# Performance work log

Measured on AMD Instinct MI355X. Metric: run time of the kernel, lower is better.

Reference implementation:

```python
import jax, jax.numpy as jnp
import numpy as np

B, N, D = 4, 2048, 512
H, DH = 8, 64  # heads, dim_head; inner_dim = H*DH = 512
SCALE = DH ** -0.5


def setup_inputs() -> dict:
    key = jax.random.key(0)
    kx, kw = jax.random.split(key)
    x = jax.random.normal(kx, (B, N, D), dtype=jnp.float32)
    # torch Linear weight layout: [out_features=3*H*DH, in_features=D]
    W_qkv = jax.random.normal(kw, (3 * H * DH, D), dtype=jnp.float32) * 0.02
    return {"x": x, "W_qkv": W_qkv}


def reference(x, W_qkv):
    b, n, d = x.shape
    # qkv projection (no bias since qkv_bias=False)
    qkv = x @ W_qkv.T                                  # [b, n, 3*H*DH]
    qkv = qkv.reshape(b, n, 3, H, DH).transpose(2, 0, 3, 1, 4)  # [3, b, H, n, DH]
    q, k, v = qkv[0], qkv[1], qkv[2]
    # shifted query: q_cross[t] = q[t-1] for t>=1, q_cross[0] = q[0]
    q_cross = jnp.concatenate([q[:, :, :1, :], q[:, :, :-1, :]], axis=2)
    scores = jnp.einsum("bhqd,bhkd->bhqk", q_cross * SCALE, k)  # [b, H, n, n]
    attn = jax.nn.softmax(scores, axis=-1)
    out = jnp.einsum("bhqk,bhkd->bhqd", attn, v)       # [b, H, n, DH]
    out = out.transpose(0, 2, 1, 3).reshape(b, n, H * DH)
    # to_out is Dropout(0.0) -> identity in eval / p=0
    return out
```

## Files before the change

kernel.cpp:

```cpp
#include <hip/hip_runtime.h>
#include <hip/hip_bf16.h>
#include <stdint.h>

typedef __bf16 bf16_t;
typedef float floatx4 __attribute__((ext_vector_type(4)));
typedef __bf16 bf16x8 __attribute__((ext_vector_type(8)));
typedef __bf16 bf16x4 __attribute__((ext_vector_type(4)));

#define QSCALE 0.1803368801111204f

__device__ __forceinline__ void gl2lds16(const bf16_t* g, bf16_t* l) {
    __builtin_amdgcn_global_load_lds(
        (const __attribute__((address_space(1))) unsigned int*)g,
        (__attribute__((address_space(3))) unsigned int*)l,
        16, 0, 0);
}

__global__ __launch_bounds__(256) void convert_kernel(const float* __restrict__ x,
                                                      bf16_t* __restrict__ xb,
                                                      const float* __restrict__ w,
                                                      bf16_t* __restrict__ wb,
                                                      int nx4) {
    int i = blockIdx.x * 256 + threadIdx.x;
    const float* in; bf16_t* out; int j;
    if (i < nx4) { in = x; out = xb; j = i; }
    else         { in = w; out = wb; j = i - nx4; }
    float4 v = ((const float4*)in)[j];
    bf16x4 o;
    o.x = (bf16_t)v.x; o.y = (bf16_t)v.y; o.z = (bf16_t)v.z; o.w = (bf16_t)v.w;
    ((bf16x4*)out)[j] = o;
}

__global__ __launch_bounds__(256) void qkv_gemm(const bf16_t* __restrict__ X,
                                                const bf16_t* __restrict__ W,
                                                bf16_t* __restrict__ Q,
                                                bf16_t* __restrict__ K,
                                                bf16_t* __restrict__ Vt)
{
    __shared__ bf16_t As[128 * 64];
    __shared__ bf16_t Bs[128 * 64];

    const int tid  = threadIdx.x;
    const int wave = tid >> 6;
    const int lane = tid & 63;
    const int quad = lane >> 4;
    const int lrow = lane & 15;
    const int t7g  = lrow & 7;
    const int bm0 = blockIdx.x * 128;
    const int bn0 = blockIdx.y * 128;
    const int mw = (wave >> 1) * 64;
    const int nw = (wave & 1) * 64;
    const int wbase = tid & 192;

    floatx4 acc[4][4];
#pragma unroll
    for (int i = 0; i < 4; i++)
#pragma unroll
        for (int j = 0; j < 4; j++) acc[i][j] = (floatx4)0.0f;

#pragma unroll 1
    for (int kb = 0; kb < 8; ++kb) {
        const int k0 = kb * 64;
        __syncthreads();
#pragma unroll
        for (int r = 0; r < 4; ++r) {
            int c = r * 256 + tid;
            int row = c >> 3, kc = c & 7;
            int skc = kc ^ (row & 7);
            gl2lds16(X + (size_t)(bm0 + row) * 512 + k0 + skc * 8,
                     As + (size_t)(r * 256 + wbase) * 8);
        }
#pragma unroll
        for (int r = 0; r < 4; ++r) {
            int c = r * 256 + tid;
            int row = c >> 3, kc = c & 7;
            int skc = kc ^ (row & 7);
            gl2lds16(W + (size_t)(bn0 + row) * 512 + k0 + skc * 8,
                     Bs + (size_t)(r * 256 + wbase) * 8);
        }
        __syncthreads();
#pragma unroll
        for (int ks = 0; ks < 2; ++ks) {
            bf16x8 af[4], bfr[4];
#pragma unroll
            for (int mi = 0; mi < 4; mi++)
                af[mi] = *(const bf16x8*)(As + (mw + mi * 16 + lrow) * 64 + (((ks * 4 + quad) ^ t7g) << 3));
#pragma unroll
            for (int ni = 0; ni < 4; ni++)
                bfr[ni] = *(const bf16x8*)(Bs + (nw + ni * 16 + lrow) * 64 + (((ks * 4 + quad) ^ t7g) << 3));
#pragma unroll
            for (int mi = 0; mi < 4; mi++)
#pragma unroll
                for (int ni = 0; ni < 4; ni++)
                    acc[mi][ni] = __builtin_amdgcn_mfma_f32_16x16x32_bf16(af[mi], bfr[ni], acc[mi][ni], 0, 0, 0);
        }
    }

#pragma unroll
    for (int mi = 0; mi < 4; mi++) {
        int mbase = bm0 + mw + mi * 16 + quad * 4;
        int b = mbase >> 11, n = mbase & 2047;
#pragma unroll
        for (int ni = 0; ni < 4; ni++) {
            int o = bn0 + nw + ni * 16 + lrow;
            int s  = o >> 9;
            int h  = (o >> 6) & 7;
            int dh = o & 63;
            int bh = b * 8 + h;
            if (s == 2) {
                bf16x4 pv;
#pragma unroll
                for (int r = 0; r < 4; r++) pv[r] = (bf16_t)acc[mi][ni][r];
                *(bf16x4*)(Vt + ((size_t)bh * 64 + dh) * 2048 + n) = pv;
            } else if (s == 0) {
#pragma unroll
                for (int r = 0; r < 4; r++)
                    Q[((size_t)bh * 2048 + n + r) * 64 + dh] = (bf16_t)(acc[mi][ni][r] * QSCALE);
            } else {
#pragma unroll
                for (int r = 0; r < 4; r++)
                    K[((size_t)bh * 2048 + n + r) * 64 + dh] = (bf16_t)acc[mi][ni][r];
            }
        }
    }
}

__device__ __forceinline__ void stage_tile(const bf16_t* __restrict__ kb,
                                           const bf16_t* __restrict__ vb,
                                           int kt, bf16_t* ksbuf, bf16_t* vsbuf,
                                           int wave, int lane) {
#pragma unroll
    for (int part = 0; part < 2; ++part) {
        int ch  = part * 256 + wave * 64 + lane;
        int row = ch >> 3, cc = ch & 7;
        int scc = cc ^ (row & 7);
        bf16_t* ldst = ksbuf + (size_t)(part * 256 + wave * 64) * 8;
        gl2lds16(kb + ((size_t)(kt * 64 + row)) * 64 + scc * 8, ldst);
        bf16_t* ldst2 = vsbuf + (size_t)(part * 256 + wave * 64) * 8;
        gl2lds16(vb + (size_t)row * 2048 + kt * 64 + scc * 8, ldst2);
    }
}

__global__ __launch_bounds__(256, 4) void flash_attn(const bf16_t* __restrict__ Q,
                                                     const bf16_t* __restrict__ K,
                                                     const bf16_t* __restrict__ Vt,
                                                     float* __restrict__ Out)
{
    __shared__ bf16_t Ks[2][64 * 64];
    __shared__ bf16_t Vs[2][64 * 64];
    __shared__ bf16_t Ps[4][32 * 32];

    const int tid  = threadIdx.x;
    const int wave = tid >> 6;
    const int lane = tid & 63;
    const int quad = lane >> 4;
    const int c    = lane & 15;
    const int t7   = c & 7;
    const int qhalf = wave >> 1;
    const int khalf = wave & 1;
    const int qt = blockIdx.x;
    const int bh = blockIdx.y;
    const int b = bh >> 3, h = bh & 7;

    bf16x8 qf[2][2];
#pragma unroll
    for (int mt = 0; mt < 2; ++mt) {
        int qg  = qt * 64 + qhalf * 32 + mt * 16 + c;
        int src = (qg == 0) ? 0 : qg - 1;
        const bf16_t* qbase = Q + ((size_t)bh * 2048 + src) * 64;
        qf[mt][0] = *(const bf16x8*)(qbase + quad * 8);
        qf[mt][1] = *(const bf16x8*)(qbase + 32 + quad * 8);
    }

    floatx4 o[2][4];
#pragma unroll
    for (int mt = 0; mt < 2; ++mt)
#pragma unroll
        for (int i = 0; i < 4; i++) o[mt][i] = (floatx4)0.0f;
    float lacc[2][4] = {{0.f, 0.f, 0.f, 0.f}, {0.f, 0.f, 0.f, 0.f}};

    const bf16_t* kb = K + ((size_t)bh * 2048) * 64;
    const bf16_t* vb = Vt + ((size_t)bh * 64) * 2048;
    bf16_t* pw = Ps[wave];

    stage_tile(kb, vb, 0, Ks[0], Vs[0], wave, lane);

#pragma unroll 1
    for (int kt = 0; kt < 32; ++kt) {
        const int buf = kt & 1;
        __syncthreads();
        if (kt < 31)
            stage_tile(kb, vb, kt + 1, Ks[buf ^ 1], Vs[buf ^ 1], wave, lane);

        const bf16_t* ks = Ks[buf];
        const bf16_t* vs = Vs[buf];

        floatx4 s[2][2];
        __builtin_amdgcn_s_setprio(1);
#pragma unroll
        for (int nt = 0; nt < 2; ++nt) {
            const bf16_t* krow = ks + (khalf * 32 + nt * 16 + c) * 64;
            bf16x8 kf0 = *(const bf16x8*)(krow + ((quad ^ t7) << 3));
            bf16x8 kf1 = *(const bf16x8*)(krow + (((4 + quad) ^ t7) << 3));
#pragma unroll
            for (int mt = 0; mt < 2; ++mt) {
                floatx4 t = (floatx4)0.0f;
                t = __builtin_amdgcn_mfma_f32_16x16x32_bf16(qf[mt][0], kf0, t, 0, 0, 0);
                t = __builtin_amdgcn_mfma_f32_16x16x32_bf16(qf[mt][1], kf1, t, 0, 0, 0);
                s[mt][nt] = t;
            }
        }
        __builtin_amdgcn_s_setprio(0);

#pragma unroll
        for (int mt = 0; mt < 2; ++mt)
#pragma unroll
            for (int nt = 0; nt < 2; ++nt)
#pragma unroll
                for (int r = 0; r < 4; r++) {
                    float p = __builtin_amdgcn_exp2f(s[mt][nt][r]);
                    lacc[mt][r] += p;
                    int row  = mt * 16 + quad * 4 + r;
                    int colc = nt * 2 + (c >> 3);
                    pw[row * 32 + ((colc ^ (row & 3)) << 3) + t7] = (bf16_t)p;
                }

        __builtin_amdgcn_s_setprio(1);
        bf16x8 pf[2];
#pragma unroll
        for (int mt = 0; mt < 2; ++mt)
            pf[mt] = *(const bf16x8*)(pw + (mt * 16 + c) * 32 + ((quad ^ (c & 3)) << 3));
#pragma unroll
        for (int sub = 0; sub < 4; ++sub) {
            const bf16_t* vrow = vs + (sub * 16 + c) * 64;
            bf16x8 vf = *(const bf16x8*)(vrow + (((khalf * 4 + quad) ^ t7) << 3));
            o[0][sub] = __builtin_amdgcn_mfma_f32_16x16x32_bf16(pf[0], vf, o[0][sub], 0, 0, 0);
            o[1][sub] = __builtin_amdgcn_mfma_f32_16x16x32_bf16(pf[1], vf, o[1][sub], 0, 0, 0);
        }
        __builtin_amdgcn_s_setprio(0);
    }

#pragma unroll
    for (int mt = 0; mt < 2; ++mt)
#pragma unroll
        for (int r = 0; r < 4; r++)
#pragma unroll
            for (int d = 1; d < 16; d <<= 1)
                lacc[mt][r] += __shfl_xor(lacc[mt][r], d, 64);

    __syncthreads();
    float* obuf = (float*)Ks;
    float* lbuf = (float*)Ps;
    if (khalf == 1) {
#pragma unroll
        for (int mt = 0; mt < 2; ++mt)
#pragma unroll
            for (int sub = 0; sub < 4; ++sub)
                *(floatx4*)(obuf + qhalf * 2048 + (mt * 4 + sub) * 256 + lane * 4) = o[mt][sub];
        if (c == 0) {
#pragma unroll
            for (int mt = 0; mt < 2; ++mt)
#pragma unroll
                for (int r = 0; r < 4; r++)
                    lbuf[qhalf * 32 + mt * 16 + quad * 4 + r] = lacc[mt][r];
        }
    }
    __syncthreads();
    if (khalf == 0) {
#pragma unroll
        for (int mt = 0; mt < 2; ++mt)
#pragma unroll
            for (int sub = 0; sub < 4; ++sub)
                o[mt][sub] += *(const floatx4*)(obuf + qhalf * 2048 + (mt * 4 + sub) * 256 + lane * 4);
#pragma unroll
        for (int mt = 0; mt < 2; ++mt)
#pragma unroll
            for (int r = 0; r < 4; r++)
                lacc[mt][r] += lbuf[qhalf * 32 + mt * 16 + quad * 4 + r];

        float* ob = Out + (size_t)b * 2048 * 512 + (size_t)h * 64;
#pragma unroll
        for (int mt = 0; mt < 2; ++mt) {
            int n0 = qt * 64 + qhalf * 32 + mt * 16 + quad * 4;
#pragma unroll
            for (int r = 0; r < 4; r++) {
                float inv = 1.0f / lacc[mt][r];
                float* orow = ob + (size_t)(n0 + r) * 512;
#pragma unroll
                for (int sub = 0; sub < 4; ++sub)
                    orow[sub * 16 + c] = o[mt][sub][r] * inv;
            }
        }
    }
}

extern "C" void kernel_launch(void* const* d_in, const int* in_sizes, int n_in,
                              void* d_out, int out_size, void* d_ws, size_t ws_size,
                              hipStream_t stream) {
    const float* x = (const float*)d_in[0];
    const float* w = (const float*)d_in[1];
    float* out = (float*)d_out;

    char* ws = (char*)d_ws;
    bf16_t* xb = (bf16_t*)(ws);
    bf16_t* wb = (bf16_t*)(ws + 8388608);
    bf16_t* q  = (bf16_t*)(ws + 9961472);
    bf16_t* k  = (bf16_t*)(ws + 18350080);
    bf16_t* vt = (bf16_t*)(ws + 26738688);

    convert_kernel<<<4864, 256, 0, stream>>>(x, xb, w, wb, 1048576);
    qkv_gemm<<<dim3(64, 12), 256, 0, stream>>>(xb, wb, q, k, vt);
    flash_attn<<<dim3(32, 32), 256, 0, stream>>>(q, k, vt, out);
}
```

Baseline: 152.9 us.

## Keep softmax probabilities in registers via transposed QK MFMA and permlane swaps

Swaps the QK^T MFMA operands so S is produced transposed, and permutes the K row order so each lane's exp2 outputs line up with the A-operand layout of the PV MFMA. A permlane32_swap finishes the exchange, so the per-wave LDS staging buffer for P and its write/read round trip go away. Row sums now stay per lane and are reduced with two cross-lane shuffles plus a broadcast at the end. The launch bound rises from 4 to 5 blocks per CU, which the freed LDS allows but which also tightens the register budget.

```diff
diff --git a/kernel.cpp b/kernel.cpp
--- a/kernel.cpp
+++ b/kernel.cpp
@@ -6,6 +6,7 @@
 typedef float floatx4 __attribute__((ext_vector_type(4)));
 typedef __bf16 bf16x8 __attribute__((ext_vector_type(8)));
 typedef __bf16 bf16x4 __attribute__((ext_vector_type(4)));
+typedef unsigned int uintx4 __attribute__((ext_vector_type(4)));
 
 #define QSCALE 0.1803368801111204f
 
@@ -14,6 +15,12 @@
         (const __attribute__((address_space(1))) unsigned int*)g,
         (__attribute__((address_space(3))) unsigned int*)l,
         16, 0, 0);
+}
+
+__device__ __forceinline__ unsigned pk2(float lo, float hi) {
+    unsigned short a = __builtin_bit_cast(unsigned short, (bf16_t)lo);
+    unsigned short b = __builtin_bit_cast(unsigned short, (bf16_t)hi);
+    return (unsigned)a | ((unsigned)b << 16);
 }
 
 __global__ __launch_bounds__(256) void convert_kernel(const float* __restrict__ x,
@@ -141,14 +148,13 @@
     }
 }
 
-__global__ __launch_bounds__(256, 4) void flash_attn(const bf16_t* __restrict__ Q,
+__global__ __launch_bounds__(256, 5) void flash_attn(const bf16_t* __restrict__ Q,
                                                      const bf16_t* __restrict__ K,
                                                      const bf16_t* __restrict__ Vt,
                                                      float* __restrict__ Out)
 {
     __shared__ bf16_t Ks[2][64 * 64];
     __shared__ bf16_t Vs[2][64 * 64];
-    __shared__ bf16_t Ps[4][32 * 32];
 
     const int tid  = threadIdx.x;
     const int wave = tid >> 6;
@@ -162,6 +168,9 @@
     const int bh = blockIdx.y;
     const int b = bh >> 3, h = bh & 7;
 
+    const int bw    = ((c & 4) << 1) | ((c & 8) >> 1) | (c & 3);
+    const int brow7 = bw & 7;
+
     bf16x8 qf[2][2];
 #pragma unroll
     for (int mt = 0; mt < 2; ++mt) {
@@ -177,11 +186,10 @@
     for (int mt = 0; mt < 2; ++mt)
 #pragma unroll
         for (int i = 0; i < 4; i++) o[mt][i] = (floatx4)0.0f;
-    float lacc[2][4] = {{0.f, 0.f, 0.f, 0.f}, {0.f, 0.f, 0.f, 0.f}};
+    float lacc[2] = {0.f, 0.f};
 
     const bf16_t* kb = K + ((size_t)bh * 2048) * 64;
     const bf16_t* vb = Vt + ((size_t)bh * 64) * 2048;
-    bf16_t* pw = Ps[wave];
 
     stage_tile(kb, vb, 0, Ks[0], Vs[0], wave, lane);
 
@@ -199,70 +207,75 @@
         __builtin_amdgcn_s_setprio(1);
 #pragma unroll
         for (int nt = 0; nt < 2; ++nt) {
-            const bf16_t* krow = ks + (khalf * 32 + nt * 16 + c) * 64;
-            bf16x8 kf0 = *(const bf16x8*)(krow + ((quad ^ t7) << 3));
-            bf16x8 kf1 = *(const bf16x8*)(krow + (((4 + quad) ^ t7) << 3));
+            const bf16_t* krow = ks + (khalf * 32 + nt * 16 + bw) * 64;
+            bf16x8 kf0 = *(const bf16x8*)(krow + ((quad ^ brow7) << 3));
+            bf16x8 kf1 = *(const bf16x8*)(krow + (((4 + quad) ^ brow7) << 3));
 #pragma unroll
             for (int mt = 0; mt < 2; ++mt) {
                 floatx4 t = (floatx4)0.0f;
-                t = __builtin_amdgcn_mfma_f32_16x16x32_bf16(qf[mt][0], kf0, t, 0, 0, 0);
-                t = __builtin_amdgcn_mfma_f32_16x16x32_bf16(qf[mt][1], kf1, t, 0, 0, 0);
+                t = __builtin_amdgcn_mfma_f32_16x16x32_bf16(kf0, qf[mt][0], t, 0, 0, 0);
+                t = __builtin_amdgcn_mfma_f32_16x16x32_bf16(kf1, qf[mt][1], t, 0, 0, 0);
                 s[mt][nt] = t;
             }
         }
         __builtin_amdgcn_s_setprio(0);
 
-#pragma unroll
-        for (int mt = 0; mt < 2; ++mt)
+        bf16x8 pfrag[2];
+#pragma unroll
+        for (int mt = 0; mt < 2; ++mt) {
+            float pe[2][4];
 #pragma unroll
             for (int nt = 0; nt < 2; ++nt)
 #pragma unroll
-                for (int r = 0; r < 4; r++) {
+                for (int r = 0; r < 4; ++r) {
                     float p = __builtin_amdgcn_exp2f(s[mt][nt][r]);
-                    lacc[mt][r] += p;
-                    int row  = mt * 16 + quad * 4 + r;
-                    int colc = nt * 2 + (c >> 3);
-                    pw[row * 32 + ((colc ^ (row & 3)) << 3) + t7] = (bf16_t)p;
+                    lacc[mt] += p;
+                    pe[nt][r] = p;
                 }
+            unsigned A0 = pk2(pe[0][0], pe[0][1]);
+            unsigned A1 = pk2(pe[0][2], pe[0][3]);
+            unsigned B0 = pk2(pe[1][0], pe[1][1]);
+            unsigned B1 = pk2(pe[1][2], pe[1][3]);
+            auto r0 = __builtin_amdgcn_permlane32_swap((int)A0, (int)B0, false, false);
+            auto r1 = __builtin_amdgcn_permlane32_swap((int)A1, (int)B1, false, false);
+            uintx4 fd;
+            fd.x = (unsigned)r0[0];
+            fd.y = (unsigned)r1[0];
+            fd.z = (unsigned)r0[1];
+            fd.w = (unsigned)r1[1];
+            pfrag[mt] = __builtin_bit_cast(bf16x8, fd);
+        }
 
         __builtin_amdgcn_s_setprio(1);
-        bf16x8 pf[2];
-#pragma unroll
-        for (int mt = 0; mt < 2; ++mt)
-            pf[mt] = *(const bf16x8*)(pw + (mt * 16 + c) * 32 + ((quad ^ (c & 3)) << 3));
 #pragma unroll
         for (int sub = 0; sub < 4; ++sub) {
             const bf16_t* vrow = vs + (sub * 16 + c) * 64;
             bf16x8 vf = *(const bf16x8*)(vrow + (((khalf * 4 + quad) ^ t7) << 3));
-            o[0][sub] = __builtin_amdgcn_mfma_f32_16x16x32_bf16(pf[0], vf, o[0][sub], 0, 0, 0);
-            o[1][sub] = __builtin_amdgcn_mfma_f32_16x16x32_bf16(pf[1], vf, o[1][sub], 0, 0, 0);
+            o[0][sub] = __builtin_amdgcn_mfma_f32_16x16x32_bf16(pfrag[0], vf, o[0][sub], 0, 0, 0);
+            o[1][sub] = __builtin_amdgcn_mfma_f32_16x16x32_bf16(pfrag[1], vf, o[1][sub], 0, 0, 0);
         }
         __builtin_amdgcn_s_setprio(0);
     }
 
 #pragma unroll
-    for (int mt = 0; mt < 2; ++mt)
-#pragma unroll
-        for (int r = 0; r < 4; r++)
-#pragma unroll
-            for (int d = 1; d < 16; d <<= 1)
-                lacc[mt][r] += __shfl_xor(lacc[mt][r], d, 64);
+    for (int mt = 0; mt < 2; ++mt) {
+        lacc[mt] += __shfl_xor(lacc[mt], 16, 64);
+        lacc[mt] += __shfl_xor(lacc[mt], 32, 64);
+    }
 
     __syncthreads();
     float* obuf = (float*)Ks;
-    float* lbuf = (float*)Ps;
+    float* lbuf = (float*)Vs;
     if (khalf == 1) {
 #pragma unroll
         for (int mt = 0; mt < 2; ++mt)
 #pragma unroll
             for (int sub = 0; sub < 4; ++sub)
                 *(floatx4*)(obuf + qhalf * 2048 + (mt * 4 + sub) * 256 + lane * 4) = o[mt][sub];
-        if (c == 0) {
+        if (lane < 16) {
 #pragma unroll
             for (int mt = 0; mt < 2; ++mt)
-#pragma unroll
-                for (int r = 0; r < 4; r++)
-                    lbuf[qhalf * 32 + mt * 16 + quad * 4 + r] = lacc[mt][r];
+                lbuf[qhalf * 32 + mt * 16 + c] = lacc[mt];
         }
     }
     __syncthreads();
@@ -274,9 +287,7 @@
                 o[mt][sub] += *(const floatx4*)(obuf + qhalf * 2048 + (mt * 4 + sub) * 256 + lane * 4);
 #pragma unroll
         for (int mt = 0; mt < 2; ++mt)
-#pragma unroll
-            for (int r = 0; r < 4; r++)
-                lacc[mt][r] += lbuf[qhalf * 32 + mt * 16 + quad * 4 + r];
+            lacc[mt] += lbuf[qhalf * 32 + mt * 16 + c];
 
         float* ob = Out + (size_t)b * 2048 * 512 + (size_t)h * 64;
 #pragma unroll
@@ -284,7 +295,8 @@
             int n0 = qt * 64 + qhalf * 32 + mt * 16 + quad * 4;
 #pragma unroll
             for (int r = 0; r < 4; r++) {
-                float inv = 1.0f / lacc[mt][r];
+                float lr = __shfl(lacc[mt], quad * 4 + r, 64);
+                float inv = 1.0f / lr;
                 float* orow = ob + (size_t)(n0 + r) * 512;
 #pragma unroll
                 for (int sub = 0; sub < 4; ++sub)
```

New measurement: 144.7 us. 5.4% less time.
